# Kernel optimization log

Measured on AMD Instinct MI355X. Metric: run time of the kernel, lower is better.

The kernel has to match this reference:

```python
import jax, jax.numpy as jnp
import numpy as np

N_ITER, N_TAPS, N_DELAY, N_SRC = 2, 4, 1, 4
EPS = 1e-3
TINY = 1e-20
BATCH, N_CHAN, N_FREQ, N_FRAMES = 2, 6, 320, 500


def mag_sq(x):
    return x.real ** 2 + x.imag ** 2


def divide(num, denom, eps):
    return num / jnp.maximum(denom, eps)


def make_xbar(X, n_taps, n_delay):
    # X: (..., c, f, n) -> X_bar: (..., c, f, t, n); tap t is X delayed by n_delay + t
    n = X.shape[-1]
    pad = [(0, 0)] * (X.ndim - 1)
    taps = [jnp.pad(X, pad + [(n_delay + t, 0)])[..., :n] for t in range(n_taps)]
    return jnp.stack(taps, axis=-2)


def background_update(W, H, C_XX, C_XbarX, eps=1e-5):
    # recompute J from W, H and input covariances (ridge-loaded solve)
    n_src = W.shape[-3]
    A1 = jnp.einsum('...sfc,...cfd->...fsd', W, C_XX)
    A2 = jnp.einsum('...sfdt,...dtfc->...fsc', H, C_XbarX)
    Am = A1 + A2
    mat = Am[..., :n_src]
    load = jnp.abs(jnp.diagonal(mat, axis1=-2, axis2=-1)).sum(axis=-1)[..., None, None]
    load = jnp.maximum(load * eps, eps) * jnp.eye(n_src, dtype=mat.dtype)
    load = jax.lax.stop_gradient(load)
    J_H = jnp.linalg.solve(mat + load, Am[..., n_src:])
    return jnp.moveaxis(J_H.conj(), -1, -3)  # (..., n_bak, f, n_src)


def iss_type1(src, Y, w, eps):
    n = Y.shape[-1]
    Ys = Y[..., src, :, :]
    vn = jnp.einsum('...cfn,...cfn,...fn->...cf', w, Y, Ys.conj()) / n
    vd = jnp.einsum('...cfn,...fn->...cf', w, mag_sq(Ys)) / n
    v = divide(vn, vd, eps)
    vs = 1.0 - 1.0 / jnp.sqrt(jnp.maximum(vd[..., src, :], eps))
    return v.at[..., src, :].set(vs.astype(v.dtype))


def iss_type2(Y, Zs, w, eps):
    vn = jnp.einsum('...cfn,...cfn,...fn->...cf', w, Y, Zs.conj())
    vd = jnp.einsum('...cfn,...fn->...cf', w, mag_sq(Zs))
    return divide(vn, vd, eps)


def iss_type3(src, tap, Y, X_bar, w, eps):
    Xst = X_bar[..., src, :, tap, :]
    vn = jnp.einsum('...cfn,...cfn,...fn->...cf', w, Y, Xst.conj())
    vd = jnp.einsum('...cfn,...fn->...cf', w, mag_sq(Xst))
    return divide(vn, vd, eps)


def mat_up1(W, H, A, v, src, eps):
    Wn = W - jnp.einsum('...cf,...fd->...cfd', v, W[..., src, :, :])
    Hn = H - jnp.einsum('...cf,...fdt->...cfdt', v, H[..., src, :, :, :])
    u = jnp.einsum('...sfc,...cf->...sf', A[..., :v.shape[-2]], v)
    u = u / (1.0 - v[..., src:src + 1, :] + eps)
    return Wn, Hn, A.at[..., src].add(u)


def mat_up2(W, J, A, v, g, eps):
    n_src = W.shape[-3]
    v2 = v[..., :n_src, :] + jnp.einsum('...sfc,...cf->...sf', W[..., n_src:], v[..., n_src:, :])
    W1 = W[..., :n_src] - jnp.einsum('...cf,...fd->...cfd', v[..., :n_src, :], g)
    Wn = jnp.concatenate([W1, W[..., n_src:]], axis=-1)
    Jn = J - jnp.einsum('...cf,...fd->...cfd', v[..., n_src:, :], g)
    Av = jnp.einsum('...sfc,...cf->...sf', A[..., :v2.shape[-2]], v2)
    gA = jnp.einsum('...fs,...sfc->...fc', g, A[..., :g.shape[-1], :, :])
    denom = 1.0 - jnp.einsum('...cf,...fc->...f', v2, gA)
    mul = denom.conj() / (mag_sq(denom) + eps)
    An = A + jnp.einsum('...sf,...fc->...sfc', Av, gA * mul[..., None])
    return Wn, Jn, An


def bak_update_vector(p, d, g, eps):
    gdg = jnp.sum(mag_sq(g) / (d + eps), axis=-2)
    gdp = jnp.sum(g.conj() * p / (d + eps), axis=-2)
    b = 1.0 - gdp
    b1 = mag_sq(b)
    a = b1 * gdg + TINY
    beta = (-b1 + jnp.sqrt(b1 ** 2 + 4.0 * a)) / (2.0 * a)
    ell1 = beta * b
    ell2 = (1.0 / jnp.sqrt(eps + gdg)).astype(ell1.dtype)
    ell = jnp.where(b1 > eps ** 2, ell1, ell2)
    return (p - ell[..., None, :] * g) / (d + eps)


def bak_update(bak, Y, Z, X, W, J, A, w, eps):
    n_src, n_freq, n_frames = Y.shape[-3:]
    n_chan = X.shape[-3]
    Zs = Z[..., bak, :, :] + X[..., n_src + bak, :, :]
    norm = 1.0 / n_frames
    ones = jnp.ones(w.shape[:-3] + (n_chan - n_src, n_freq, n_frames), w.dtype)
    wz = jnp.concatenate([w, ones], axis=-3)
    YZ = jnp.concatenate([Y, Z], axis=-3)
    p = jnp.einsum('...cfn,...cfn,...fn->...cf', YZ, wz, Zs.conj()) * norm
    d = jnp.einsum('...cfn,...fn->...cf', wz, mag_sq(Zs)) * norm
    A2 = jnp.concatenate([A, jnp.einsum('...sfc,...cfd->...sfd', A, W[..., n_src:])], axis=-1)
    g = jnp.einsum('...fs,...sfc->...cf', J[..., bak, :, :], A2).conj()
    v = bak_update_vector(p, d, g, eps)
    YZ = YZ - jnp.einsum('...cf,...fn->...cfn', v, Zs)
    return v, YZ[..., :n_src, :, :], YZ[..., n_src:, :, :]


def iss_updates(Y, X, X_bar, W, H, A, w, J, Z, eps):
    n_src = Y.shape[-3]
    n_chan = X.shape[-3]
    n_taps = X_bar.shape[-2]
    n_bak = n_chan - n_src
    # 1) background rows (structured type-2 updates)
    for bak in range(n_bak):
        v, Y, Z = bak_update(bak, Y, Z, X, W, J, A, w, eps)
        g = J[..., bak, :, :]
        W, J, A = mat_up2(W, J, A, v, g, eps)
    # 2) source directions (type 1)
    for src in range(n_src):
        v = iss_type1(src, Y, w, eps)
        Y = Y - jnp.einsum('...cf,...fn->...cfn', v, Y[..., src, :, :])
        W, H, A = mat_up1(W, H, A, v, src, eps)
    # 3) background directions (type 2)
    for bak in range(n_bak):
        v = iss_type2(Y, Z[..., bak, :, :], w, eps)
        Y = Y - jnp.einsum('...cf,...fn->...cfn', v, Z[..., bak, :, :])
        W = W.at[..., :n_src].add(-jnp.einsum('...cf,...fd->...cfd', v, J[..., bak, :, :]))
        W = W.at[..., n_src + bak].add(v)
    if n_bak > 0:
        # keep A consistent: A = inv(W1 + W2 J) per frequency
        Binv = W[..., :n_src] + jnp.einsum('...sfc,...cfd->...sfd', W[..., n_src:], J)
        A = jnp.moveaxis(jnp.linalg.inv(jnp.moveaxis(Binv, -2, -3)), -3, -2)
    # 4) dereverberation taps (type 3)
    for src in range(n_chan):
        for tap in range(n_taps):
            v = iss_type3(src, tap, Y, X_bar, w, eps)
            Y = Y - jnp.einsum('...cf,...fn->...cfn', v, X_bar[..., src, :, tap, :])
            H = H.at[..., src, tap].add(v)
    return Y, Z, W, H, J, A


def _forward(X):
    batch = X.shape[:-3]
    n_chan, n_freq, n_frames = X.shape[-3:]
    n_src = N_SRC
    X_bar = make_xbar(X, N_TAPS, N_DELAY)
    W = jnp.broadcast_to(jnp.eye(n_src, n_chan, dtype=X.dtype)[:, None, :], batch + (n_src, n_freq, n_chan))
    H = jnp.zeros(batch + (n_src, n_freq, n_chan, N_TAPS), X.dtype)
    A = jnp.broadcast_to(jnp.eye(n_src, dtype=X.dtype)[:, None, :], batch + (n_src, n_freq, n_src))
    # initialize background demixing J from input second-order statistics
    C_XX = jnp.einsum('...cfn,...dfn->...cfd', X, X.conj()) / n_frames
    C_XbarX = jnp.einsum('...dftn,...cfn->...dtfc', X_bar, X.conj()) / n_frames
    J = background_update(W, H, C_XX, C_XbarX)
    Y = X[..., :n_src, :, :]
    Z = jnp.einsum('...cfd,...dfn->...cfn', J, X[..., :n_src, :, :]) - X[..., n_src:, :, :]
    for _ in range(N_ITER):
        # Gauss (time-varying) source-model weights, shared across frequencies
        w = 1.0 / jnp.maximum(jnp.mean(mag_sq(Y), axis=-2, keepdims=True), EPS)
        w = jnp.broadcast_to(w, Y.shape)
        Y, Z, W, H, J, A = iss_updates(Y, X, X_bar, W, H, A, w, J, Z, EPS)
    return Y


def setup_inputs():
    key = jax.random.key(0)
    k1, k2 = jax.random.split(key)
    shape = (BATCH, N_CHAN, N_FREQ, N_FRAMES)
    return {"X_real": jax.random.normal(k1, shape, jnp.float32),
            "X_imag": jax.random.normal(k2, shape, jnp.float32)}


def reference(X_real, X_imag):
    X = jax.lax.complex(X_real, X_imag)
    return _forward(X)
```

## Files before the change

kernel.cpp:

```cpp
#include <hip/hip_runtime.h>

#define NFR 500
#define NFQ 320
#define NB  2
#define NC  6
#define NS  4
#define NBK 2
#define NT  4
#define NDLY 1
#define EPSF 1e-3f
#define TINYF 1e-20f

#define NP   512
#define XPAD 8
#define XLEN (XPAD + NP)
#define NCH  8
#define FPC  (NFQ / NCH)

typedef float f2 __attribute__((ext_vector_type(2)));

__device__ __forceinline__ f2 mk2(float r, float i){ f2 t; t.x = r; t.y = i; return t; }
__device__ __forceinline__ f2 cmul(f2 a, f2 b){ return a.xx*b + a.yy*mk2(-b.y, b.x); }
__device__ __forceinline__ f2 cmulc(f2 a, f2 b){ return b.xx*a + b.yy*mk2(a.y, -a.x); }
__device__ __forceinline__ f2 conjc(f2 a){ return mk2(a.x, -a.y); }
__device__ __forceinline__ float cmag2(f2 a){ return a.x*a.x + a.y*a.y; }
__device__ __forceinline__ f2 cinv(f2 a){ float m = a.x*a.x + a.y*a.y; return mk2(a.x/m, -a.y/m); }

#define DPPF(x, ctrl) __int_as_float(__builtin_amdgcn_mov_dpp(__float_as_int(x), (ctrl), 0xF, 0xF, true))
__device__ __forceinline__ float wred64(float x){
  x += DPPF(x, 0x111);
  x += DPPF(x, 0x112);
  x += DPPF(x, 0x114);
  x += DPPF(x, 0x118);
  x += DPPF(x, 0x142);
  x += DPPF(x, 0x143);
  return __int_as_float(__builtin_amdgcn_readlane(__float_as_int(x), 63));
}

__global__ __launch_bounds__(256) void k_init(
  const float* __restrict__ Xr, const float* __restrict__ Xi,
  f2* __restrict__ Yg, f2* __restrict__ Zg,
  f2* __restrict__ Wg, f2* __restrict__ Jg, f2* __restrict__ Ag)
{
  __shared__ f2 sX[NC][NFR];
  __shared__ f2 sC[NS][NC];
  __shared__ f2 sJl[NBK][NS];

  const int bf = blockIdx.x;
  const int b = bf / NFQ, f = bf % NFQ;
  const int tid = threadIdx.x, wv = tid >> 6, lane = tid & 63;

  for (int c = 0; c < NC; ++c) {
    const size_t base = ((size_t)(b*NC + c)*NFQ + f)*NFR;
    for (int n = tid; n < NFR; n += 256)
      sX[c][n] = mk2(Xr[base+n], Xi[base+n]);
  }
  __syncthreads();

  for (int p = wv; p < NS*NC; p += 4) {
    int s = p / NC, d = p % NC;
    f2 ar2 = mk2(0.f,0.f), ai2 = mk2(0.f,0.f);
    for (int n = lane; n < NFR; n += 64) {
      f2 xs = sX[s][n], xd = sX[d][n];
      ar2 += xs * xd;
      ai2 += xs.yx * mk2(xd.x, -xd.y);
    }
    float ar = wred64(ar2.x + ar2.y), ai = wred64(ai2.x + ai2.y);
    if (lane == 0) sC[s][d] = mk2(ar*(1.f/NFR), ai*(1.f/NFR));
  }
  __syncthreads();

  if (tid == 0) {
    f2 M[NS][NC];
    for (int s = 0; s < NS; ++s)
      for (int d = 0; d < NC; ++d) M[s][d] = sC[s][d];
    float dsum = 0.f;
    for (int s = 0; s < NS; ++s) dsum += sqrtf(cmag2(M[s][s]));
    float load = fmaxf(dsum*1e-5f, 1e-5f);
    for (int s = 0; s < NS; ++s) M[s][s].x += load;
    for (int col = 0; col < NS; ++col) {
      int piv = col; float best = cmag2(M[col][col]);
      for (int r = col+1; r < NS; ++r) { float m = cmag2(M[r][col]); if (m > best){best=m; piv=r;} }
      if (piv != col) for (int k = 0; k < NC; ++k) { f2 t=M[col][k]; M[col][k]=M[piv][k]; M[piv][k]=t; }
      f2 ip = cinv(M[col][col]);
      for (int k = col; k < NC; ++k) M[col][k] = cmul(M[col][k], ip);
      for (int r = 0; r < NS; ++r) if (r != col) {
        f2 fac = M[r][col];
        for (int k = col; k < NC; ++k) M[r][k] -= cmul(fac, M[col][k]);
      }
    }
    for (int k = 0; k < NBK; ++k)
      for (int s = 0; s < NS; ++s) sJl[k][s] = conjc(M[s][NS+k]);
  }
  __syncthreads();

  if (tid < NBK*NS) {
    int k = tid / NS, s = tid % NS;
    Jg[((size_t)(b*NBK+k)*NFQ + f)*NS + s] = sJl[k][s];
  } else if (tid < NBK*NS + NS*NC) {
    int t = tid - NBK*NS; int s = t / NC, d = t % NC;
    Wg[((size_t)(b*NS+s)*NFQ + f)*NC + d] = (s==d) ? mk2(1.f,0.f) : mk2(0.f,0.f);
  } else if (tid < NBK*NS + NS*NC + NS*NS) {
    int t = tid - NBK*NS - NS*NC; int s = t / NS, d = t % NS;
    Ag[((size_t)(b*NS+s)*NFQ + f)*NS + d] = (s==d) ? mk2(1.f,0.f) : mk2(0.f,0.f);
  }
  for (int c = 0; c < NS; ++c) {
    const size_t base = ((size_t)(b*NS + c)*NFQ + f)*NFR;
    for (int n = tid; n < NFR; n += 256) Yg[base+n] = sX[c][n];
  }
  for (int k = 0; k < NBK; ++k) {
    const size_t base = ((size_t)(b*NBK + k)*NFQ + f)*NFR;
    for (int n = tid; n < NFR; n += 256) {
      f2 acc = -sX[NS+k][n];
      for (int s = 0; s < NS; ++s) acc += cmul(sJl[k][s], sX[s][n]);
      Zg[base+n] = acc;
    }
  }
}

__global__ __launch_bounds__(512) void k_wpart(const f2* __restrict__ Yg,
                                               float* __restrict__ wacc)
{
  const int bs = blockIdx.x / NCH;
  const int ch = blockIdx.x % NCH;
  const int n  = threadIdx.x;
  if (n >= NFR) return;
  const f2* row = Yg + (size_t)bs*NFQ*NFR;
  f2 acc2 = mk2(0.f,0.f);
  for (int ff = 0; ff < FPC; ++ff) {
    f2 y = row[(size_t)(ch*FPC + ff)*NFR + n];
    acc2 += y*y;
  }
  wacc[((size_t)(ch*NB*NS + bs))*NFR + n] = acc2.x + acc2.y;
}

__global__ __launch_bounds__(256, 4) void k_iter(
  const float* __restrict__ Xr, const float* __restrict__ Xi,
  f2* __restrict__ Yg, f2* __restrict__ Zg,
  f2* __restrict__ Wg, f2* __restrict__ Jg, f2* __restrict__ Ag,
  const float* __restrict__ wacc, float* __restrict__ outR, const int last)
{
  __shared__ f2 sXp[NC][XLEN];
  __shared__ f2 sZ[NBK][NP];
  __shared__ f2 sS[NP];
  __shared__ f2 sW[NS][NC];
  __shared__ f2 sJ[NBK][NS];
  __shared__ f2 sA[NS][NS];
  __shared__ f2 sB[NS][2*NS];
  __shared__ f2 sv[NC], sg[NC], sgo[NS], sp[NC];
  __shared__ float sd[NC];
  __shared__ f2 sAv[NS], sgA[NS], sWsrc[NC];

  const int bf = blockIdx.x;
  const int b = bf / NFQ, f = bf % NFQ;
  const int tid = threadIdx.x, wv = tid >> 6, lane = tid & 63;

  f2 yreg[8];
  float wreg[8];

  for (int c = 0; c < NC; ++c) {
    const size_t base = ((size_t)(b*NC + c)*NFQ + f)*NFR;
    for (int j = tid; j < XLEN; j += 256) {
      int n = j - XPAD;
      sXp[c][j] = (n >= 0 && n < NFR) ? mk2(Xr[base+n], Xi[base+n]) : mk2(0.f,0.f);
    }
  }
  for (int k = 0; k < NBK; ++k) {
    const size_t zb = ((size_t)(b*NBK + k)*NFQ + f)*NFR;
    for (int n = tid; n < NP; n += 256) sZ[k][n] = (n < NFR) ? Zg[zb+n] : mk2(0.f,0.f);
  }
  {
    const size_t yb = ((size_t)(b*NS + wv)*NFQ + f)*NFR;
    const int bs = b*NS + wv;
#pragma unroll
    for (int i = 0; i < 8; ++i) {
      int n = lane + 64*i;
      if (n < NFR) {
        yreg[i] = Yg[yb+n];
        float a = 0.f;
#pragma unroll
        for (int ch = 0; ch < NCH; ++ch) a += wacc[((size_t)(ch*NB*NS + bs))*NFR + n];
        wreg[i] = 1.0f / fmaxf(a * (1.0f/(float)NFQ), EPSF);
      } else { yreg[i] = mk2(0.f,0.f); wreg[i] = 0.f; }
    }
  }
  if (tid < NS*NC) sW[tid/NC][tid%NC] = Wg[((size_t)(b*NS + tid/NC)*NFQ + f)*NC + tid%NC];
  else if (tid < NS*NC + NBK*NS) { int t=tid-NS*NC; sJ[t/NS][t%NS] = Jg[((size_t)(b*NBK+t/NS)*NFQ+f)*NS + t%NS]; }
  else if (tid < NS*NC + NBK*NS + NS*NS) { int t=tid-NS*NC-NBK*NS; sA[t/NS][t%NS] = Ag[((size_t)(b*NS+t/NS)*NFQ+f)*NS + t%NS]; }
  __syncthreads();

  f2 vloc[NC];

  for (int bak = 0; bak < NBK; ++bak) {
    for (int n = tid; n < NP; n += 256)
      sS[n] = sZ[bak][n] + sXp[NS+bak][XPAD+n];
    if (bak > 0 && tid < 16) {
      int s = tid >> 2, c = tid & 3;
      f2 v2[NS];
#pragma unroll
      for (int t = 0; t < NS; ++t)
        v2[t] = vloc[t] + cmul(sW[t][NS+0], vloc[NS+0]) + cmul(sW[t][NS+1], vloc[NS+1]);
      f2 den = mk2(1.f,0.f);
#pragma unroll
      for (int cc = 0; cc < NS; ++cc) den -= cmul(v2[cc], sgA[cc]);
      float m2 = cmag2(den) + EPSF;
      f2 mul = mk2(den.x/m2, -den.y/m2);
      sA[s][c] += cmul(sAv[s], cmul(sgA[c], mul));
    }
    __syncthreads();

    f2 zs[8];
    {
      f2 pr2 = mk2(0.f,0.f), pi2 = mk2(0.f,0.f), dd2 = mk2(0.f,0.f);
#pragma unroll
      for (int i = 0; i < 8; ++i) {
        zs[i] = sS[lane+64*i];
        f2 wy = wreg[i]*yreg[i];
        pr2 += wy * zs[i];
        pi2 += wy.yx * mk2(zs[i].x, -zs[i].y);
        dd2 += (wreg[i]*zs[i]) * zs[i];
      }
      float pr = wred64(pr2.x+pr2.y), pi = wred64(pi2.x+pi2.y), dd = wred64(dd2.x+dd2.y);
      if (lane == 0) { sp[wv] = mk2(pr*(1.f/NFR), pi*(1.f/NFR)); sd[wv] = dd*(1.f/NFR); }
      if (wv < NBK) {
        f2 qr2 = mk2(0.f,0.f), qi2 = mk2(0.f,0.f), qd2 = mk2(0.f,0.f);
#pragma unroll
        for (int i = 0; i < 8; ++i) {
          f2 y = sZ[wv][lane+64*i];
          qr2 += y * zs[i];
          qi2 += y.yx * mk2(zs[i].x, -zs[i].y);
          qd2 += zs[i]*zs[i];
        }
        float qr = wred64(qr2.x+qr2.y), qi = wred64(qi2.x+qi2.y), qd = wred64(qd2.x+qd2.y);
        if (lane == 0) { sp[NS+wv] = mk2(qr*(1.f/NFR), qi*(1.f/NFR)); sd[NS+wv] = qd*(1.f/NFR); }
      }
    }
    if (tid < NC) {
      int c = tid; f2 acc = mk2(0.f,0.f);
      for (int s = 0; s < NS; ++s) {
        f2 a2;
        if (c < NS) a2 = sA[s][c];
        else {
          a2 = mk2(0.f,0.f);
          for (int k = 0; k < NS; ++k) a2 += cmul(sA[s][k], sW[k][c]);
        }
        acc += cmul(sJ[bak][s], a2);
      }
      sg[c] = conjc(acc);
    } else if (tid >= 8 && tid < 8+NS) {
      sgo[tid-8] = sJ[bak][tid-8];
    }
    __syncthreads();

    {
      float gdg = 0.f; f2 gdp = mk2(0.f,0.f);
#pragma unroll
      for (int c = 0; c < NC; ++c) {
        f2 gc = sg[c]; float id = 1.0f/(sd[c] + EPSF);
        gdg += cmag2(gc) * id;
        gdp += id * cmulc(sp[c], gc);
      }
      f2 bb = mk2(1.0f - gdp.x, -gdp.y);
      float b1 = cmag2(bb);
      float a = b1*gdg + TINYF;
      float beta = (-b1 + sqrtf(b1*b1 + 4.0f*a)) / (2.0f*a);
      f2 ell = (b1 > EPSF*EPSF) ? (beta*bb) : mk2(1.0f/sqrtf(EPSF + gdg), 0.f);
#pragma unroll
      for (int c = 0; c < NC; ++c)
        vloc[c] = (1.0f/(sd[c] + EPSF)) * (sp[c] - cmul(ell, sg[c]));
    }
    {
      f2 vc = vloc[wv];
#pragma unroll
      for (int i = 0; i < 8; ++i) yreg[i] -= cmul(vc, zs[i]);
      if (wv < NBK) {
        f2 v2c = vloc[NS+wv];
#pragma unroll
        for (int i = 0; i < 8; ++i) sZ[wv][lane+64*i] -= cmul(v2c, zs[i]);
      }
    }
    __syncthreads();

    if (tid < NS) {
      f2 v2[NS];
#pragma unroll
      for (int t = 0; t < NS; ++t)
        v2[t] = vloc[t] + cmul(sW[t][NS+0], vloc[NS+0]) + cmul(sW[t][NS+1], vloc[NS+1]);
      f2 acc = mk2(0.f,0.f);
#pragma unroll
      for (int c = 0; c < NS; ++c) acc += cmul(sA[tid][c], v2[c]);
      sAv[tid] = acc;
    } else if (tid < 2*NS) {
      int c = tid - NS; f2 acc = mk2(0.f,0.f);
#pragma unroll
      for (int s = 0; s < NS; ++s) acc += cmul(sgo[s], sA[s][c]);
      sgA[c] = acc;
    } else if (tid < 2*NS + 16) {
      int idx = tid - 2*NS; int cc = idx >> 2, d = idx & 3;
      sW[cc][d] -= cmul(vloc[cc], sgo[d]);
    } else if (tid < 2*NS + 16 + 8) {
      int idx = tid - 2*NS - 16; int k = idx >> 2, d = idx & 3;
      sJ[k][d] -= cmul(vloc[NS+k], sgo[d]);
    }
    __syncthreads();
  }

  for (int src = 0; src < NS; ++src) {
    if (wv == src) {
#pragma unroll
      for (int i = 0; i < 8; ++i) sS[lane+64*i] = yreg[i];
    }
    if (tid < NC) sWsrc[tid] = sW[src][tid];
    if (src == 0) {
      if (tid < 16) {
        int s = tid >> 2, c = tid & 3;
        f2 v2[NS];
#pragma unroll
        for (int t = 0; t < NS; ++t)
          v2[t] = vloc[t] + cmul(sW[t][NS+0], vloc[NS+0]) + cmul(sW[t][NS+1], vloc[NS+1]);
        f2 den = mk2(1.f,0.f);
#pragma unroll
        for (int cc = 0; cc < NS; ++cc) den -= cmul(v2[cc], sgA[cc]);
        float m2 = cmag2(den) + EPSF;
        f2 mul = mk2(den.x/m2, -den.y/m2);
        sA[s][c] += cmul(sAv[s], cmul(sgA[c], mul));
      }
    } else if (tid >= 8 && tid < 8+NS) {
      int r = tid - 8, prev = src - 1;
      f2 acc = mk2(0.f,0.f);
#pragma unroll
      for (int c = 0; c < NS; ++c) acc += cmul(sA[r][c], sv[c]);
      float den = 1.0f - sv[prev].x + EPSF;
      sA[r][prev] += (1.0f/den) * acc;
    }
    __syncthreads();

    {
      f2 ys[8];
      f2 nr2 = mk2(0.f,0.f), ni2 = mk2(0.f,0.f), dd2 = mk2(0.f,0.f);
#pragma unroll
      for (int i = 0; i < 8; ++i) {
        ys[i] = sS[lane+64*i];
        f2 wy = wreg[i]*yreg[i];
        nr2 += wy * ys[i];
        ni2 += wy.yx * mk2(ys[i].x, -ys[i].y);
        dd2 += (wreg[i]*ys[i]) * ys[i];
      }
      float nr = wred64(nr2.x+nr2.y)*(1.f/NFR);
      float ni = wred64(ni2.x+ni2.y)*(1.f/NFR);
      float dd = wred64(dd2.x+dd2.y)*(1.f/NFR);
      f2 vc;
      if (wv == src) vc = mk2(1.0f - 1.0f/sqrtf(fmaxf(dd, EPSF)), 0.f);
      else           vc = (1.0f/fmaxf(dd, EPSF)) * mk2(nr, ni);
      if (lane == 0) sv[wv] = vc;
#pragma unroll
      for (int i = 0; i < 8; ++i) yreg[i] -= cmul(vc, ys[i]);
      if (lane < NC) sW[wv][lane] -= cmul(vc, sWsrc[lane]);
    }
    __syncthreads();
  }

  {
    f2 pr0=mk2(0,0), pi0=mk2(0,0), dd0=mk2(0,0);
    f2 pr1=mk2(0,0), pi1=mk2(0,0), dd1=mk2(0,0);
    f2 crr=mk2(0,0), cri=mk2(0,0);
    f2 z0c[8], z1c[8];
#pragma unroll
    for (int i = 0; i < 8; ++i) {
      f2 z0 = sZ[0][lane+64*i], z1 = sZ[1][lane+64*i];
      z0c[i] = z0; z1c[i] = z1;
      f2 wy = wreg[i]*yreg[i];
      f2 wz0 = wreg[i]*z0;
      pr0 += wy * z0;  pi0 += wy.yx * mk2(z0.x, -z0.y);  dd0 += wz0 * z0;
      pr1 += wy * z1;  pi1 += wy.yx * mk2(z1.x, -z1.y);  dd1 += (wreg[i]*z1) * z1;
      crr += wz0 * z1; cri += wz0.yx * mk2(z1.x, -z1.y);
    }
    float P0r = wred64(pr0.x+pr0.y), P0i = wred64(pi0.x+pi0.y), D0 = wred64(dd0.x+dd0.y);
    float P1r = wred64(pr1.x+pr1.y), P1i = wred64(pi1.x+pi1.y), D1 = wred64(dd1.x+dd1.y);
    float Rr  = wred64(crr.x+crr.y), Ri  = wred64(cri.x+cri.y);
    f2 v0 = (1.0f/fmaxf(D0, EPSF)) * mk2(P0r, P0i);
    f2 P1c = mk2(P1r, P1i) - cmul(v0, mk2(Rr, Ri));
    f2 v1 = (1.0f/fmaxf(D1, EPSF)) * P1c;
#pragma unroll
    for (int i = 0; i < 8; ++i) yreg[i] -= cmul(v0, z0c[i]) + cmul(v1, z1c[i]);
    if (lane < NS) sW[wv][lane] -= cmul(v0, sJ[0][lane]) + cmul(v1, sJ[1][lane]);
    else if (lane == NS)   sW[wv][NS+0] += v0;
    else if (lane == NS+1) sW[wv][NS+1] += v1;
  }
  __syncthreads();

  if (tid < 16) {
    int s = tid >> 2, d = tid & 3;
    f2 acc = sW[s][d];
    acc += cmul(sW[s][NS+0], sJ[0][d]);
    acc += cmul(sW[s][NS+1], sJ[1][d]);
    sB[s][d] = acc;
    sB[s][NS+d] = (s==d) ? mk2(1.f,0.f) : mk2(0.f,0.f);
  }
  __syncthreads();
  if (tid == 0) {
    for (int col = 0; col < NS; ++col) {
      int piv = col; float best = cmag2(sB[col][col]);
      for (int r = col+1; r < NS; ++r) { float m = cmag2(sB[r][col]); if (m > best) { best = m; piv = r; } }
      if (piv != col) for (int k = 0; k < 2*NS; ++k) { f2 t = sB[col][k]; sB[col][k] = sB[piv][k]; sB[piv][k] = t; }
      f2 ip = cinv(sB[col][col]);
      for (int k = 0; k < 2*NS; ++k) sB[col][k] = cmul(sB[col][k], ip);
      for (int r = 0; r < NS; ++r) if (r != col) {
        f2 fac = sB[r][col];
        for (int k = 0; k < 2*NS; ++k) sB[r][k] -= cmul(fac, sB[col][k]);
      }
    }
  }

  {
#pragma unroll 1
    for (int src = 0; src < NC; ++src) {
      const f2* __restrict__ xrow = &sXp[src][0];
#pragma unroll
      for (int tap = 0; tap < NT; ++tap) {
        const int xoff = XPAD - (NDLY + tap) + lane;
        f2 xs[8];
        f2 nr2 = mk2(0.f,0.f), ni2 = mk2(0.f,0.f), dd2 = mk2(0.f,0.f);
#pragma unroll
        for (int i = 0; i < 8; ++i) {
          xs[i] = xrow[xoff + 64*i];
          f2 wy = wreg[i]*yreg[i];
          nr2 += wy * xs[i];
          ni2 += wy.yx * mk2(xs[i].x, -xs[i].y);
          dd2 += (wreg[i]*xs[i]) * xs[i];
        }
        float nr = wred64(nr2.x+nr2.y), ni = wred64(ni2.x+ni2.y), dd = wred64(dd2.x+dd2.y);
        f2 vc = (1.0f/fmaxf(dd, EPSF)) * mk2(nr, ni);
#pragma unroll
        for (int i = 0; i < 8; ++i) yreg[i] -= cmul(vc, xs[i]);
      }
    }
  }

  {
    const size_t yb = ((size_t)(b*NS + wv)*NFQ + f)*NFR;
    if (last) {
#pragma unroll
      for (int i = 0; i < 8; ++i) { int n = lane+64*i; if (n < NFR) outR[yb+n] = yreg[i].x; }
    } else {
#pragma unroll
      for (int i = 0; i < 8; ++i) { int n = lane+64*i; if (n < NFR) Yg[yb+n] = yreg[i]; }
    }
  }
  if (!last) {
    __syncthreads();
    for (int k = 0; k < NBK; ++k) {
      const size_t zb = ((size_t)(b*NBK+k)*NFQ + f)*NFR;
      for (int n = tid; n < NFR; n += 256) Zg[zb+n] = sZ[k][n];
    }
    if (tid < NS*NC) Wg[((size_t)(b*NS + tid/NC)*NFQ + f)*NC + tid%NC] = sW[tid/NC][tid%NC];
    else if (tid < NS*NC + NBK*NS) { int t = tid - NS*NC; Jg[((size_t)(b*NBK + t/NS)*NFQ + f)*NS + t%NS] = sJ[t/NS][t%NS]; }
    else if (tid < NS*NC + NBK*NS + NS*NS) { int t = tid - NS*NC - NBK*NS; Ag[((size_t)(b*NS + t/NS)*NFQ + f)*NS + t%NS] = sB[t/NS][NS + t%NS]; }
  }
}

extern "C" void kernel_launch(void* const* d_in, const int* in_sizes, int n_in,
                              void* d_out, int out_size, void* d_ws, size_t ws_size,
                              hipStream_t stream)
{
  (void)in_sizes; (void)n_in; (void)out_size; (void)ws_size;
  const float* Xr = (const float*)d_in[0];
  const float* Xi = (const float*)d_in[1];
  float* outR = (float*)d_out;

  char* ws = (char*)d_ws;
  size_t off = 0;
  f2* Yg = (f2*)(ws + off); off += (size_t)NB*NS*NFQ*NFR*sizeof(f2);
  f2* Zg = (f2*)(ws + off); off += (size_t)NB*NBK*NFQ*NFR*sizeof(f2);
  f2* Wg = (f2*)(ws + off); off += (size_t)NB*NS*NFQ*NC*sizeof(f2);
  f2* Jg = (f2*)(ws + off); off += (size_t)NB*NBK*NFQ*NS*sizeof(f2);
  f2* Ag = (f2*)(ws + off); off += (size_t)NB*NS*NFQ*NS*sizeof(f2);
  float* wacc = (float*)(ws + off); off += (size_t)NCH*NB*NS*NFR*sizeof(float);

  k_init<<<NB*NFQ, 256, 0, stream>>>(Xr, Xi, Yg, Zg, Wg, Jg, Ag);
  for (int it = 0; it < 2; ++it) {
    k_wpart<<<NB*NS*NCH, 512, 0, stream>>>(Yg, wacc);
    k_iter<<<NB*NFQ, 256, 0, stream>>>(Xr, Xi, Yg, Zg, Wg, Jg, Ag, wacc, outR, it == 1);
  }
}
```

Before: 136.4 us.

## Fuse init into first iteration kernel and compute first weights from X directly

Removes the separate k_init kernel. The covariance, ridge-loaded solve for J, Z computation and identity W/A setup now run inside the first k_iter launch, reusing the X tile already staged in shared memory. The first weight partials are computed directly from X (Y equals the first source channels at that point), so Y and Z no longer make a round trip through global memory before iteration one. It also skips the trailing 4x4 inversion on the last iteration. This saves one launch and a large amount of global traffic, at the cost of longer serial setup on thread 0 inside the iteration kernel.

```diff
diff --git a/kernel.cpp b/kernel.cpp
--- a/kernel.cpp
+++ b/kernel.cpp
@@ -37,85 +37,23 @@
   return __int_as_float(__builtin_amdgcn_readlane(__float_as_int(x), 63));
 }
 
-__global__ __launch_bounds__(256) void k_init(
-  const float* __restrict__ Xr, const float* __restrict__ Xi,
-  f2* __restrict__ Yg, f2* __restrict__ Zg,
-  f2* __restrict__ Wg, f2* __restrict__ Jg, f2* __restrict__ Ag)
+__global__ __launch_bounds__(512) void k_wpartX(const float* __restrict__ Xr,
+                                                const float* __restrict__ Xi,
+                                                float* __restrict__ wacc)
 {
-  __shared__ f2 sX[NC][NFR];
-  __shared__ f2 sC[NS][NC];
-  __shared__ f2 sJl[NBK][NS];
-
-  const int bf = blockIdx.x;
-  const int b = bf / NFQ, f = bf % NFQ;
-  const int tid = threadIdx.x, wv = tid >> 6, lane = tid & 63;
-
-  for (int c = 0; c < NC; ++c) {
-    const size_t base = ((size_t)(b*NC + c)*NFQ + f)*NFR;
-    for (int n = tid; n < NFR; n += 256)
-      sX[c][n] = mk2(Xr[base+n], Xi[base+n]);
-  }
-  __syncthreads();
-
-  for (int p = wv; p < NS*NC; p += 4) {
-    int s = p / NC, d = p % NC;
-    f2 ar2 = mk2(0.f,0.f), ai2 = mk2(0.f,0.f);
-    for (int n = lane; n < NFR; n += 64) {
-      f2 xs = sX[s][n], xd = sX[d][n];
-      ar2 += xs * xd;
-      ai2 += xs.yx * mk2(xd.x, -xd.y);
-    }
-    float ar = wred64(ar2.x + ar2.y), ai = wred64(ai2.x + ai2.y);
-    if (lane == 0) sC[s][d] = mk2(ar*(1.f/NFR), ai*(1.f/NFR));
-  }
-  __syncthreads();
-
-  if (tid == 0) {
-    f2 M[NS][NC];
-    for (int s = 0; s < NS; ++s)
-      for (int d = 0; d < NC; ++d) M[s][d] = sC[s][d];
-    float dsum = 0.f;
-    for (int s = 0; s < NS; ++s) dsum += sqrtf(cmag2(M[s][s]));
-    float load = fmaxf(dsum*1e-5f, 1e-5f);
-    for (int s = 0; s < NS; ++s) M[s][s].x += load;
-    for (int col = 0; col < NS; ++col) {
-      int piv = col; float best = cmag2(M[col][col]);
-      for (int r = col+1; r < NS; ++r) { float m = cmag2(M[r][col]); if (m > best){best=m; piv=r;} }
-      if (piv != col) for (int k = 0; k < NC; ++k) { f2 t=M[col][k]; M[col][k]=M[piv][k]; M[piv][k]=t; }
-      f2 ip = cinv(M[col][col]);
-      for (int k = col; k < NC; ++k) M[col][k] = cmul(M[col][k], ip);
-      for (int r = 0; r < NS; ++r) if (r != col) {
-        f2 fac = M[r][col];
-        for (int k = col; k < NC; ++k) M[r][k] -= cmul(fac, M[col][k]);
-      }
-    }
-    for (int k = 0; k < NBK; ++k)
-      for (int s = 0; s < NS; ++s) sJl[k][s] = conjc(M[s][NS+k]);
-  }
-  __syncthreads();
-
-  if (tid < NBK*NS) {
-    int k = tid / NS, s = tid % NS;
-    Jg[((size_t)(b*NBK+k)*NFQ + f)*NS + s] = sJl[k][s];
-  } else if (tid < NBK*NS + NS*NC) {
-    int t = tid - NBK*NS; int s = t / NC, d = t % NC;
-    Wg[((size_t)(b*NS+s)*NFQ + f)*NC + d] = (s==d) ? mk2(1.f,0.f) : mk2(0.f,0.f);
-  } else if (tid < NBK*NS + NS*NC + NS*NS) {
-    int t = tid - NBK*NS - NS*NC; int s = t / NS, d = t % NS;
-    Ag[((size_t)(b*NS+s)*NFQ + f)*NS + d] = (s==d) ? mk2(1.f,0.f) : mk2(0.f,0.f);
-  }
-  for (int c = 0; c < NS; ++c) {
-    const size_t base = ((size_t)(b*NS + c)*NFQ + f)*NFR;
-    for (int n = tid; n < NFR; n += 256) Yg[base+n] = sX[c][n];
-  }
-  for (int k = 0; k < NBK; ++k) {
-    const size_t base = ((size_t)(b*NBK + k)*NFQ + f)*NFR;
-    for (int n = tid; n < NFR; n += 256) {
-      f2 acc = -sX[NS+k][n];
-      for (int s = 0; s < NS; ++s) acc += cmul(sJl[k][s], sX[s][n]);
-      Zg[base+n] = acc;
-    }
-  }
+  const int bs = blockIdx.x / NCH;
+  const int ch = blockIdx.x % NCH;
+  const int n  = threadIdx.x;
+  if (n >= NFR) return;
+  const int b = bs / NS, s = bs % NS;
+  const size_t rowb = ((size_t)(b*NC + s)*NFQ)*NFR;
+  float acc = 0.f;
+  for (int ff = 0; ff < FPC; ++ff) {
+    size_t idx = rowb + (size_t)(ch*FPC + ff)*NFR + n;
+    float xr = Xr[idx], xi = Xi[idx];
+    acc += xr*xr + xi*xi;
+  }
+  wacc[((size_t)(ch*NB*NS + bs))*NFR + n] = acc;
 }
 
 __global__ __launch_bounds__(512) void k_wpart(const f2* __restrict__ Yg,
@@ -138,7 +76,8 @@
   const float* __restrict__ Xr, const float* __restrict__ Xi,
   f2* __restrict__ Yg, f2* __restrict__ Zg,
   f2* __restrict__ Wg, f2* __restrict__ Jg, f2* __restrict__ Ag,
-  const float* __restrict__ wacc, float* __restrict__ outR, const int last)
+  const float* __restrict__ wacc, float* __restrict__ outR,
+  const int first, const int last)
 {
   __shared__ f2 sXp[NC][XLEN];
   __shared__ f2 sZ[NBK][NP];
@@ -147,8 +86,9 @@
   __shared__ f2 sJ[NBK][NS];
   __shared__ f2 sA[NS][NS];
   __shared__ f2 sB[NS][2*NS];
-  __shared__ f2 sv[NC], sg[NC], sgo[NS], sp[NC];
+  __shared__ f2 sv[NC], sg[NC], sgo[NS];
   __shared__ float sd[NC];
+  __shared__ f2 sp[NC];
   __shared__ f2 sAv[NS], sgA[NS], sWsrc[NC];
 
   const int bf = blockIdx.x;
@@ -165,29 +105,101 @@
       sXp[c][j] = (n >= 0 && n < NFR) ? mk2(Xr[base+n], Xi[base+n]) : mk2(0.f,0.f);
     }
   }
-  for (int k = 0; k < NBK; ++k) {
-    const size_t zb = ((size_t)(b*NBK + k)*NFQ + f)*NFR;
-    for (int n = tid; n < NP; n += 256) sZ[k][n] = (n < NFR) ? Zg[zb+n] : mk2(0.f,0.f);
-  }
-  {
-    const size_t yb = ((size_t)(b*NS + wv)*NFQ + f)*NFR;
-    const int bs = b*NS + wv;
-#pragma unroll
-    for (int i = 0; i < 8; ++i) {
-      int n = lane + 64*i;
-      if (n < NFR) {
-        yreg[i] = Yg[yb+n];
-        float a = 0.f;
-#pragma unroll
-        for (int ch = 0; ch < NCH; ++ch) a += wacc[((size_t)(ch*NB*NS + bs))*NFR + n];
-        wreg[i] = 1.0f / fmaxf(a * (1.0f/(float)NFQ), EPSF);
-      } else { yreg[i] = mk2(0.f,0.f); wreg[i] = 0.f; }
-    }
-  }
-  if (tid < NS*NC) sW[tid/NC][tid%NC] = Wg[((size_t)(b*NS + tid/NC)*NFQ + f)*NC + tid%NC];
-  else if (tid < NS*NC + NBK*NS) { int t=tid-NS*NC; sJ[t/NS][t%NS] = Jg[((size_t)(b*NBK+t/NS)*NFQ+f)*NS + t%NS]; }
-  else if (tid < NS*NC + NBK*NS + NS*NS) { int t=tid-NS*NC-NBK*NS; sA[t/NS][t%NS] = Ag[((size_t)(b*NS+t/NS)*NFQ+f)*NS + t%NS]; }
-  __syncthreads();
+
+  if (first) {
+    __syncthreads();
+    for (int p = wv; p < NS*NC; p += 4) {
+      int s = p / NC, d = p % NC;
+      f2 ar2 = mk2(0.f,0.f), ai2 = mk2(0.f,0.f);
+#pragma unroll
+      for (int i = 0; i < 8; ++i) {
+        int n = lane + 64*i;
+        f2 xs = sXp[s][XPAD+n], xd = sXp[d][XPAD+n];
+        ar2 += xs * xd;
+        ai2 += xs.yx * mk2(xd.x, -xd.y);
+      }
+      float ar = wred64(ar2.x + ar2.y), ai = wred64(ai2.x + ai2.y);
+      if (lane == 0) sB[s][d] = mk2(ar*(1.f/NFR), ai*(1.f/NFR));
+    }
+    if (tid >= 192 && tid < 192 + NS*NC) {
+      int t = tid - 192; sW[t/NC][t%NC] = (t/NC == t%NC) ? mk2(1.f,0.f) : mk2(0.f,0.f);
+    } else if (tid >= 224 && tid < 224 + NS*NS) {
+      int t = tid - 224; sA[t/NS][t%NS] = (t/NS == t%NS) ? mk2(1.f,0.f) : mk2(0.f,0.f);
+    }
+    __syncthreads();
+    if (tid == 0) {
+      f2 M[NS][NC];
+      for (int s = 0; s < NS; ++s)
+        for (int d = 0; d < NC; ++d) M[s][d] = sB[s][d];
+      float dsum = 0.f;
+      for (int s = 0; s < NS; ++s) dsum += sqrtf(cmag2(M[s][s]));
+      float load = fmaxf(dsum*1e-5f, 1e-5f);
+      for (int s = 0; s < NS; ++s) M[s][s].x += load;
+      for (int col = 0; col < NS; ++col) {
+        int piv = col; float best = cmag2(M[col][col]);
+        for (int r = col+1; r < NS; ++r) { float m = cmag2(M[r][col]); if (m > best){best=m; piv=r;} }
+        if (piv != col) for (int k = 0; k < NC; ++k) { f2 t=M[col][k]; M[col][k]=M[piv][k]; M[piv][k]=t; }
+        f2 ip = cinv(M[col][col]);
+        for (int k = col; k < NC; ++k) M[col][k] = cmul(M[col][k], ip);
+        for (int r = 0; r < NS; ++r) if (r != col) {
+          f2 fac = M[r][col];
+          for (int k = col; k < NC; ++k) M[r][k] -= cmul(fac, M[col][k]);
+        }
+      }
+      for (int k = 0; k < NBK; ++k)
+        for (int s = 0; s < NS; ++s) sJ[k][s] = conjc(M[s][NS+k]);
+    }
+    __syncthreads();
+    for (int n = tid; n < NP; n += 256) {
+      f2 x0 = sXp[0][XPAD+n], x1 = sXp[1][XPAD+n], x2 = sXp[2][XPAD+n], x3 = sXp[3][XPAD+n];
+      f2 a0 = -sXp[NS+0][XPAD+n];
+      a0 += cmul(sJ[0][0], x0); a0 += cmul(sJ[0][1], x1);
+      a0 += cmul(sJ[0][2], x2); a0 += cmul(sJ[0][3], x3);
+      f2 a1 = -sXp[NS+1][XPAD+n];
+      a1 += cmul(sJ[1][0], x0); a1 += cmul(sJ[1][1], x1);
+      a1 += cmul(sJ[1][2], x2); a1 += cmul(sJ[1][3], x3);
+      sZ[0][n] = a0; sZ[1][n] = a1;
+    }
+    {
+      const int bs = b*NS + wv;
+#pragma unroll
+      for (int i = 0; i < 8; ++i) {
+        int n = lane + 64*i;
+        yreg[i] = sXp[wv][XPAD+n];
+        if (n < NFR) {
+          float a = 0.f;
+#pragma unroll
+          for (int cc = 0; cc < NCH; ++cc) a += wacc[((size_t)(cc*NB*NS + bs))*NFR + n];
+          wreg[i] = 1.0f / fmaxf(a * (1.0f/(float)NFQ), EPSF);
+        } else wreg[i] = 0.f;
+      }
+    }
+    __syncthreads();
+  } else {
+    for (int k = 0; k < NBK; ++k) {
+      const size_t zb = ((size_t)(b*NBK + k)*NFQ + f)*NFR;
+      for (int n = tid; n < NP; n += 256) sZ[k][n] = (n < NFR) ? Zg[zb+n] : mk2(0.f,0.f);
+    }
+    {
+      const size_t yb = ((size_t)(b*NS + wv)*NFQ + f)*NFR;
+      const int bs = b*NS + wv;
+#pragma unroll
+      for (int i = 0; i < 8; ++i) {
+        int n = lane + 64*i;
+        if (n < NFR) {
+          yreg[i] = Yg[yb+n];
+          float a = 0.f;
+#pragma unroll
+          for (int cc = 0; cc < NCH; ++cc) a += wacc[((size_t)(cc*NB*NS + bs))*NFR + n];
+          wreg[i] = 1.0f / fmaxf(a * (1.0f/(float)NFQ), EPSF);
+        } else { yreg[i] = mk2(0.f,0.f); wreg[i] = 0.f; }
+      }
+    }
+    if (tid < NS*NC) sW[tid/NC][tid%NC] = Wg[((size_t)(b*NS + tid/NC)*NFQ + f)*NC + tid%NC];
+    else if (tid < NS*NC + NBK*NS) { int t=tid-NS*NC; sJ[t/NS][t%NS] = Jg[((size_t)(b*NBK+t/NS)*NFQ+f)*NS + t%NS]; }
+    else if (tid < NS*NC + NBK*NS + NS*NS) { int t=tid-NS*NC-NBK*NS; sA[t/NS][t%NS] = Ag[((size_t)(b*NS+t/NS)*NFQ+f)*NS + t%NS]; }
+    __syncthreads();
+  }
 
   f2 vloc[NC];
 
@@ -389,25 +401,27 @@
   }
   __syncthreads();
 
-  if (tid < 16) {
-    int s = tid >> 2, d = tid & 3;
-    f2 acc = sW[s][d];
-    acc += cmul(sW[s][NS+0], sJ[0][d]);
-    acc += cmul(sW[s][NS+1], sJ[1][d]);
-    sB[s][d] = acc;
-    sB[s][NS+d] = (s==d) ? mk2(1.f,0.f) : mk2(0.f,0.f);
-  }
-  __syncthreads();
-  if (tid == 0) {
-    for (int col = 0; col < NS; ++col) {
-      int piv = col; float best = cmag2(sB[col][col]);
-      for (int r = col+1; r < NS; ++r) { float m = cmag2(sB[r][col]); if (m > best) { best = m; piv = r; } }
-      if (piv != col) for (int k = 0; k < 2*NS; ++k) { f2 t = sB[col][k]; sB[col][k] = sB[piv][k]; sB[piv][k] = t; }
-      f2 ip = cinv(sB[col][col]);
-      for (int k = 0; k < 2*NS; ++k) sB[col][k] = cmul(sB[col][k], ip);
-      for (int r = 0; r < NS; ++r) if (r != col) {
-        f2 fac = sB[r][col];
-        for (int k = 0; k < 2*NS; ++k) sB[r][k] -= cmul(fac, sB[col][k]);
+  if (!last) {
+    if (tid < 16) {
+      int s = tid >> 2, d = tid & 3;
+      f2 acc = sW[s][d];
+      acc += cmul(sW[s][NS+0], sJ[0][d]);
+      acc += cmul(sW[s][NS+1], sJ[1][d]);
+      sB[s][d] = acc;
+      sB[s][NS+d] = (s==d) ? mk2(1.f,0.f) : mk2(0.f,0.f);
+    }
+    __syncthreads();
+    if (tid == 0) {
+      for (int col = 0; col < NS; ++col) {
+        int piv = col; float best = cmag2(sB[col][col]);
+        for (int r = col+1; r < NS; ++r) { float m = cmag2(sB[r][col]); if (m > best) { best = m; piv = r; } }
+        if (piv != col) for (int k = 0; k < 2*NS; ++k) { f2 t = sB[col][k]; sB[col][k] = sB[piv][k]; sB[piv][k] = t; }
+        f2 ip = cinv(sB[col][col]);
+        for (int k = 0; k < 2*NS; ++k) sB[col][k] = cmul(sB[col][k], ip);
+        for (int r = 0; r < NS; ++r) if (r != col) {
+          f2 fac = sB[r][col];
+          for (int k = 0; k < 2*NS; ++k) sB[r][k] -= cmul(fac, sB[col][k]);
+        }
       }
     }
   }
@@ -477,9 +491,8 @@
   f2* Ag = (f2*)(ws + off); off += (size_t)NB*NS*NFQ*NS*sizeof(f2);
   float* wacc = (float*)(ws + off); off += (size_t)NCH*NB*NS*NFR*sizeof(float);
 
-  k_init<<<NB*NFQ, 256, 0, stream>>>(Xr, Xi, Yg, Zg, Wg, Jg, Ag);
-  for (int it = 0; it < 2; ++it) {
-    k_wpart<<<NB*NS*NCH, 512, 0, stream>>>(Yg, wacc);
-    k_iter<<<NB*NFQ, 256, 0, stream>>>(Xr, Xi, Yg, Zg, Wg, Jg, Ag, wacc, outR, it == 1);
-  }
+  k_wpartX<<<NB*NS*NCH, 512, 0, stream>>>(Xr, Xi, wacc);
+  k_iter<<<NB*NFQ, 256, 0, stream>>>(Xr, Xi, Yg, Zg, Wg, Jg, Ag, wacc, outR, 1, 0);
+  k_wpart<<<NB*NS*NCH, 512, 0, stream>>>(Yg, wacc);
+  k_iter<<<NB*NFQ, 256, 0, stream>>>(Xr, Xi, Yg, Zg, Wg, Jg, Ag, wacc, outR, 0, 1);
 }
```

After: 119.1 us. 12.7% less time.
